# Kernel optimization log

Hardware: AMD Instinct MI355X
Metric: run time of the kernel (lower is better)

Reference implementation:

```python
import jax, jax.numpy as jnp
import numpy as np

EMBED = 1024
HEADS = 16
HEAD_DIM = EMBED // HEADS
BATCH = 2
SEQ = 256

def setup_inputs() -> dict:
    key = jax.random.key(0)
    ks = jax.random.split(key, 6)
    x = jax.random.normal(ks[0], (BATCH, SEQ, EMBED), dtype=jnp.float32)
    s = 1.0 / np.sqrt(HEAD_DIM)
    Wq = jax.random.uniform(ks[1], (HEAD_DIM, HEAD_DIM), jnp.float32, -s, s)
    Wk = jax.random.uniform(ks[2], (HEAD_DIM, HEAD_DIM), jnp.float32, -s, s)
    Wv = jax.random.uniform(ks[3], (HEAD_DIM, HEAD_DIM), jnp.float32, -s, s)
    so = 1.0 / np.sqrt(EMBED)
    Wo = jax.random.uniform(ks[4], (EMBED, EMBED), jnp.float32, -so, so)
    bo = jax.random.uniform(ks[5], (EMBED,), jnp.float32, -so, so)
    return {"x": x, "Wq": Wq, "Wk": Wk, "Wv": Wv, "Wo": Wo, "bo": bo}

def reference(x, Wq, Wk, Wv, Wo, bo):
    n, s, e = x.shape
    xr = x.reshape(n, s, HEADS, HEAD_DIM)          # (n,s,h,d)
    # nn.Linear applies x @ W.T
    q = jnp.einsum('nshd,ed->nshe', xr, Wq)
    k = jnp.einsum('nshd,ed->nshe', xr, Wk)
    v = jnp.einsum('nshd,ed->nshe', xr, Wv)
    # elementwise outer-product score: (n,s,t,h,d), no reduction over d
    energy = q[:, :, None, :, :] * k[:, None, :, :, :]
    # NOTE: original code softmaxes over dim=3 == the HEADS axis
    attn = jax.nn.softmax(energy / jnp.float32(np.sqrt(EMBED)), axis=3)
    out = jnp.einsum('nsthd,nthd->nshd', attn, v)  # reduce over t
    out = out.reshape(n, s, HEADS * HEAD_DIM)
    return out @ Wo.T + bo
```

## Files before the change

kernel.cpp:

```cpp
#include <hip/hip_runtime.h>

#define NB 2
#define SQL 256
#define NH 16
#define HD 64
#define EMB 1024

typedef unsigned short ushortT;
typedef unsigned int uintT;
typedef __attribute__((ext_vector_type(8))) short bf16x8;
typedef __attribute__((ext_vector_type(4))) float f32x4;
typedef __attribute__((ext_vector_type(2))) float f32x2;

__device__ __constant__ float kQSCALE = 1.4426950408889634f / 32.0f;

__device__ __forceinline__ float fexp2(float x) { return __builtin_amdgcn_exp2f(x); }
__device__ __forceinline__ float frcp(float x)  { return __builtin_amdgcn_rcpf(x); }

__device__ __forceinline__ ushortT f2bf(float x) {
    uintT u = __float_as_uint(x);
    u += 0x7fffu + ((u >> 16) & 1u);
    return (ushortT)(u >> 16);
}
__device__ __forceinline__ ushort4 f2bf4(float4 a) {
    return make_ushort4(f2bf(a.x), f2bf(a.y), f2bf(a.z), f2bf(a.w));
}
__device__ __forceinline__ f32x2 unpk2(uintT u) {
    f32x2 r;
    r.x = __uint_as_float(u << 16);
    r.y = __uint_as_float(u & 0xffff0000u);
    return r;
}
__device__ __forceinline__ float pairsum_dpp(float u) {
    const int j = __builtin_amdgcn_mov_dpp(__float_as_int(u), 0xB1, 0xF, 0xF, true);
    return u + __int_as_float(j);
}

__global__ __launch_bounds__(256) void qkv_kernel(
    const float* __restrict__ x,
    const float* __restrict__ Wq,
    const float* __restrict__ Wk,
    const float* __restrict__ Wv,
    const float* __restrict__ Wo,
    ushortT* __restrict__ Q,
    ushortT* __restrict__ K,
    ushortT* __restrict__ V,
    float* __restrict__ AO,
    ushortT* __restrict__ Wob)
{
    __shared__ ushortT wls[3][64 * 72];
    __shared__ ushortT xs[2][16 * 72];

    const int tid = threadIdx.x;
    const int ns0 = blockIdx.x * 2;
    const int g   = blockIdx.x * 256 + tid;

    {
        const float4 z = make_float4(0.f, 0.f, 0.f, 0.f);
        ((float4*)AO)[g] = z;
        ((float4*)AO)[g + 65536] = z;
    }
#pragma unroll
    for (int j = 0; j < 4; ++j) {
        const int f4 = j * 65536 + g;
        ((ushort4*)Wob)[f4] = f2bf4(((const float4*)Wo)[f4]);
    }

#pragma unroll
    for (int m = 0; m < 3; ++m) {
        const float4* src = (m == 0) ? (const float4*)Wq
                          : (m == 1) ? (const float4*)Wk : (const float4*)Wv;
#pragma unroll
        for (int j = 0; j < 4; ++j) {
            const int idx = j * 256 + tid;
            const int e   = idx >> 4;
            const int d4  = idx & 15;
            float4 a = src[idx];
            if (m == 0) { a.x *= kQSCALE; a.y *= kQSCALE; a.z *= kQSCALE; a.w *= kQSCALE; }
            *(ushort4*)&wls[m][e * 72 + d4 * 4] = f2bf4(a);
        }
    }
#pragma unroll
    for (int j = 0; j < 2; ++j) {
        const int idx = j * 256 + tid;
        const int r   = idx >> 8;
        const int h   = (idx >> 4) & 15;
        const int d4  = idx & 15;
        const float4 a = ((const float4*)(x + (size_t)(ns0 + r) * EMB))[idx & 255];
        *(ushort4*)&xs[r][h * 72 + d4 * 4] = f2bf4(a);
    }
    __syncthreads();

    const int w   = tid >> 6;
    const int nsr = w >> 1;
    const int eb0 = (w & 1) * 32;
    const int l   = tid & 63;
    const int lr  = l & 15;
    const int lk  = l >> 4;

    const bf16x8 a0 = *(const bf16x8*)&xs[nsr][lr * 72 + lk * 8];
    const bf16x8 a1 = *(const bf16x8*)&xs[nsr][lr * 72 + 32 + lk * 8];

#pragma unroll
    for (int m = 0; m < 3; ++m) {
        ushortT* outp = (m == 0) ? Q : (m == 1) ? K : V;
#pragma unroll
        for (int ef = 0; ef < 2; ++ef) {
            const int eb = eb0 + ef * 16;
            const bf16x8 b0 = *(const bf16x8*)&wls[m][(eb + lr) * 72 + lk * 8];
            const bf16x8 b1 = *(const bf16x8*)&wls[m][(eb + lr) * 72 + 32 + lk * 8];
            f32x4 c = {0.f, 0.f, 0.f, 0.f};
            c = __builtin_amdgcn_mfma_f32_16x16x32_bf16(a0, b0, c, 0, 0, 0);
            c = __builtin_amdgcn_mfma_f32_16x16x32_bf16(a1, b1, c, 0, 0, 0);
            ushortT* dst = outp + (size_t)(ns0 + nsr) * EMB + (eb + lr) * 16 + lk * 4;
            *(ushort4*)dst = make_ushort4(f2bf(c[0]), f2bf(c[1]), f2bf(c[2]), f2bf(c[3]));
        }
    }
}

#define ATTN_STEP(KU4, VU4)                                                    \
    {                                                                          \
        f32x2 k2[4], v2[4], p0[4], p1[4];                                      \
        k2[0] = unpk2(KU4.x); k2[1] = unpk2(KU4.y);                            \
        k2[2] = unpk2(KU4.z); k2[3] = unpk2(KU4.w);                            \
        _Pragma("unroll")                                                      \
        for (int j = 0; j < 4; ++j) {                                          \
            const f32x2 x0 = q0_2[j] * k2[j];                                  \
            const f32x2 x1 = q1_2[j] * k2[j];                                  \
            p0[j].x = fexp2(x0.x); p0[j].y = fexp2(x0.y);                      \
            p1[j].x = fexp2(x1.x); p1[j].y = fexp2(x1.y);                      \
        }                                                                      \
        const f32x2 s0v = (p0[0] + p0[1]) + (p0[2] + p0[3]);                   \
        const f32x2 s1v = (p1[0] + p1[1]) + (p1[2] + p1[3]);                   \
        const float rs0 = frcp(pairsum_dpp(s0v.x + s0v.y));                    \
        const float rs1 = frcp(pairsum_dpp(s1v.x + s1v.y));                    \
        const f32x2 rb0 = {rs0, rs0};                                          \
        const f32x2 rb1 = {rs1, rs1};                                          \
        v2[0] = unpk2(VU4.x); v2[1] = unpk2(VU4.y);                            \
        v2[2] = unpk2(VU4.z); v2[3] = unpk2(VU4.w);                            \
        _Pragma("unroll")                                                      \
        for (int j = 0; j < 4; ++j) {                                          \
            acc0[j] = __builtin_elementwise_fma(v2[j] * rb0, p0[j], acc0[j]);  \
            acc1[j] = __builtin_elementwise_fma(v2[j] * rb1, p1[j], acc1[j]);  \
        }                                                                      \
    }

__global__ __launch_bounds__(256) void attn_kernel(
    const ushortT* __restrict__ Q,
    const ushortT* __restrict__ K,
    const ushortT* __restrict__ V,
    float* __restrict__ AO)
{
    __shared__ float red[16][256];

    const int b    = blockIdx.x;
    const int tw   = b & 1;
    const int eh   = (b >> 1) & 1;
    const int sg   = (b >> 2) & 127;
    const int n    = b >> 9;
    const int wave = threadIdx.x >> 6;
    const int l    = threadIdx.x & 63;
    const int s0   = sg * 2;
    const int t0   = tw * 128 + wave * 32;

    f32x2 q0_2[4], q1_2[4];
    {
        const uint4* qp = (const uint4*)(Q + (size_t)(n * SQL + s0) * EMB + 512 * eh) + l;
        const uint4 qa = qp[0];
        const uint4 qb = qp[128];
        q0_2[0] = unpk2(qa.x); q0_2[1] = unpk2(qa.y);
        q0_2[2] = unpk2(qa.z); q0_2[3] = unpk2(qa.w);
        q1_2[0] = unpk2(qb.x); q1_2[1] = unpk2(qb.y);
        q1_2[2] = unpk2(qb.z); q1_2[3] = unpk2(qb.w);
    }

    f32x2 acc0[4], acc1[4];
#pragma unroll
    for (int j = 0; j < 4; ++j) {
        acc0[j] = (f32x2){0.f, 0.f};
        acc1[j] = (f32x2){0.f, 0.f};
    }

    const uint4* kp = (const uint4*)(K + (size_t)(n * SQL + t0) * EMB + 512 * eh) + l;
    const uint4* vp = (const uint4*)(V + (size_t)(n * SQL + t0) * EMB + 512 * eh) + l;

    uint4 ka = kp[0];
    uint4 kb = kp[128];
    uint4 va = vp[0];

#pragma unroll
    for (int tt = 0; tt < 30; tt += 2) {
        const uint4 kn2 = kp[256];
        const uint4 vb  = vp[128];
        ATTN_STEP(ka, va);
        const uint4 kn3 = kp[384];
        va = vp[256];
        kp += 256; vp += 256;
        ATTN_STEP(kb, vb);
        ka = kn2; kb = kn3;
    }
    {
        const uint4 vb = vp[128];
        ATTN_STEP(ka, va);
        ATTN_STEP(kb, vb);
    }

#pragma unroll
    for (int j = 0; j < 4; ++j) {
        red[2 * j        ][wave * 64 + l] = acc0[j].x;
        red[2 * j + 1    ][wave * 64 + l] = acc0[j].y;
        red[8 + 2 * j    ][wave * 64 + l] = acc1[j].x;
        red[8 + 2 * j + 1][wave * 64 + l] = acc1[j].y;
    }
    __syncthreads();

    float* aob = AO + (size_t)(n * SQL + s0) * EMB + 512 * (l & 1) + 32 * eh + (l >> 1);
#pragma unroll
    for (int di = 0; di < 4; ++di) {
        const int i = wave * 4 + di;
        const float sum = (red[i][l] + red[i][64 + l]) + (red[i][128 + l] + red[i][192 + l]);
        const int s = i >> 3;
        const int c = i & 7;
        atomicAdd(aob + (size_t)s * EMB + 64 * c, sum);
    }
}

__global__ __launch_bounds__(256) void proj_kernel(
    const float* __restrict__ AO,
    const ushortT* __restrict__ Wob,
    const float* __restrict__ bo,
    float* __restrict__ out)
{
    __shared__ ushortT As[32 * 40];
    __shared__ ushortT Bs[64 * 40];

    const int b  = blockIdx.x;
    const int jt = b & 15;
    const int rt = b >> 4;
    const int tid = threadIdx.x;
    const int r0 = rt * 32, j0 = jt * 64;

    const int w  = tid >> 6;
    const int wr = w >> 1;
    const int wc = w & 1;
    const int l  = tid & 63;
    const int lr = l & 15;
    const int lk = l >> 4;

    const int arow = tid >> 3, akq = tid & 7;
    const int brow = tid >> 2, bko = tid & 3;

    f32x4 c0 = {0.f, 0.f, 0.f, 0.f};
    f32x4 c1 = {0.f, 0.f, 0.f, 0.f};

    float4 aN = *(const float4*)&AO[(size_t)(r0 + arow) * EMB + akq * 4];
    uint4  bN = *(const uint4*)&Wob[(size_t)(j0 + brow) * EMB + bko * 8];

    for (int kt = 0; kt < 32; ++kt) {
        __syncthreads();
        *(ushort4*)&As[arow * 40 + akq * 4] = f2bf4(aN);
        *(uint4*)&Bs[brow * 40 + bko * 8] = bN;
        if (kt < 31) {
            const int kb = (kt + 1) * 32;
            aN = *(const float4*)&AO[(size_t)(r0 + arow) * EMB + kb + akq * 4];
            bN = *(const uint4*)&Wob[(size_t)(j0 + brow) * EMB + kb + bko * 8];
        }
        __syncthreads();

        const bf16x8 a  = *(const bf16x8*)&As[(wr * 16 + lr) * 40 + lk * 8];
        const bf16x8 b0 = *(const bf16x8*)&Bs[(wc * 32 + lr) * 40 + lk * 8];
        const bf16x8 b1 = *(const bf16x8*)&Bs[(wc * 32 + 16 + lr) * 40 + lk * 8];
        c0 = __builtin_amdgcn_mfma_f32_16x16x32_bf16(a, b0, c0, 0, 0, 0);
        c1 = __builtin_amdgcn_mfma_f32_16x16x32_bf16(a, b1, c1, 0, 0, 0);
    }

    const int rbase = r0 + wr * 16 + lk * 4;
    const int jbase = j0 + wc * 32 + lr;
    const float bb0 = bo[jbase];
    const float bb1 = bo[jbase + 16];
#pragma unroll
    for (int e = 0; e < 4; ++e) {
        out[(size_t)(rbase + e) * EMB + jbase]      = c0[e] + bb0;
        out[(size_t)(rbase + e) * EMB + jbase + 16] = c1[e] + bb1;
    }
}

extern "C" void kernel_launch(void* const* d_in, const int* in_sizes, int n_in,
                              void* d_out, int out_size, void* d_ws, size_t ws_size,
                              hipStream_t stream)
{
    const float* x  = (const float*)d_in[0];
    const float* Wq = (const float*)d_in[1];
    const float* Wk = (const float*)d_in[2];
    const float* Wv = (const float*)d_in[3];
    const float* Wo = (const float*)d_in[4];
    const float* bo = (const float*)d_in[5];

    float* ws = (float*)d_ws;
    ushortT* Q   = (ushortT*)ws;
    ushortT* K   = (ushortT*)(ws + 262144);
    ushortT* V   = (ushortT*)(ws + 524288);
    float*   AO  = ws + 786432;
    ushortT* Wob = (ushortT*)(ws + 1310720);

    qkv_kernel<<<256, 256, 0, stream>>>(x, Wq, Wk, Wv, Wo, Q, K, V, AO, Wob);
    attn_kernel<<<1024, 256, 0, stream>>>(Q, K, V, AO);
    proj_kernel<<<256, 256, 0, stream>>>(AO, Wob, bo, (float*)d_out);
}
```

Before: 50.26 us.

## Stage K/V tiles in shared memory shared across waves handling different query rows

Each block now has its four waves handle different query-row pairs over the same 32-key chunk. K/V tiles of 8 rows are staged into double-buffered LDS with register prefetch, so the block reads each K/V row from global memory once instead of once per wave. The per-block LDS reduction is removed: each wave atomically adds its partial sums directly. This raises the global atomic count about fourfold (8 key-chunk blocks instead of 2 per output) and adds LDS traffic plus a barrier per tile, in exchange for less global K/V traffic.

```diff
diff --git a/kernel.cpp b/kernel.cpp
--- a/kernel.cpp
+++ b/kernel.cpp
@@ -151,17 +151,18 @@
     const ushortT* __restrict__ V,
     float* __restrict__ AO)
 {
-    __shared__ float red[16][256];
+    __shared__ ushortT kv[2 * 2 * 8 * 512];
 
     const int b    = blockIdx.x;
-    const int tw   = b & 1;
-    const int eh   = (b >> 1) & 1;
-    const int sg   = (b >> 2) & 127;
+    const int tw   = b & 7;
+    const int eh   = (b >> 3) & 1;
+    const int sg   = (b >> 4) & 31;
     const int n    = b >> 9;
-    const int wave = threadIdx.x >> 6;
-    const int l    = threadIdx.x & 63;
-    const int s0   = sg * 2;
-    const int t0   = tw * 128 + wave * 32;
+    const int tid  = threadIdx.x;
+    const int wave = tid >> 6;
+    const int l    = tid & 63;
+    const int s0   = sg * 8 + wave * 2;
+    const int tB   = tw * 32;
 
     f32x2 q0_2[4], q1_2[4];
     {
@@ -181,47 +182,47 @@
         acc1[j] = (f32x2){0.f, 0.f};
     }
 
-    const uint4* kp = (const uint4*)(K + (size_t)(n * SQL + t0) * EMB + 512 * eh) + l;
-    const uint4* vp = (const uint4*)(V + (size_t)(n * SQL + t0) * EMB + 512 * eh) + l;
-
-    uint4 ka = kp[0];
-    uint4 kb = kp[128];
-    uint4 va = vp[0];
-
-#pragma unroll
-    for (int tt = 0; tt < 30; tt += 2) {
-        const uint4 kn2 = kp[256];
-        const uint4 vb  = vp[128];
-        ATTN_STEP(ka, va);
-        const uint4 kn3 = kp[384];
-        va = vp[256];
-        kp += 256; vp += 256;
-        ATTN_STEP(kb, vb);
-        ka = kn2; kb = kn3;
-    }
-    {
-        const uint4 vb = vp[128];
-        ATTN_STEP(ka, va);
-        ATTN_STEP(kb, vb);
-    }
-
+    const ushortT* Kb = K + (size_t)(n * SQL + tB) * EMB + 512 * eh + l * 8;
+    const ushortT* Vb = V + (size_t)(n * SQL + tB) * EMB + 512 * eh + l * 8;
+    const int rA = wave, rB = 4 + wave;
+
+    uint4 sk0 = *(const uint4*)&Kb[(size_t)rA * EMB];
+    uint4 sk1 = *(const uint4*)&Kb[(size_t)rB * EMB];
+    uint4 sv0 = *(const uint4*)&Vb[(size_t)rA * EMB];
+    uint4 sv1 = *(const uint4*)&Vb[(size_t)rB * EMB];
+
+#pragma unroll
+    for (int tile = 0; tile < 4; ++tile) {
+        const int buf = tile & 1;
+        ushortT* kbuf = &kv[(buf * 2 + 0) * 8 * 512];
+        ushortT* vbuf = &kv[(buf * 2 + 1) * 8 * 512];
+        *(uint4*)&kbuf[rA * 512 + l * 8] = sk0;
+        *(uint4*)&kbuf[rB * 512 + l * 8] = sk1;
+        *(uint4*)&vbuf[rA * 512 + l * 8] = sv0;
+        *(uint4*)&vbuf[rB * 512 + l * 8] = sv1;
+        __syncthreads();
+        if (tile < 3) {
+            const size_t off = (size_t)(tile + 1) * 8 * EMB;
+            sk0 = *(const uint4*)&Kb[off + (size_t)rA * EMB];
+            sk1 = *(const uint4*)&Kb[off + (size_t)rB * EMB];
+            sv0 = *(const uint4*)&Vb[off + (size_t)rA * EMB];
+            sv1 = *(const uint4*)&Vb[off + (size_t)rB * EMB];
+        }
+#pragma unroll
+        for (int t = 0; t < 8; ++t) {
+            const uint4 ku = *(const uint4*)&kbuf[t * 512 + l * 8];
+            const uint4 vu = *(const uint4*)&vbuf[t * 512 + l * 8];
+            ATTN_STEP(ku, vu);
+        }
+    }
+
+    float* aob = AO + (size_t)(n * SQL + s0) * EMB + 512 * (l & 1) + 32 * eh + (l >> 1);
 #pragma unroll
     for (int j = 0; j < 4; ++j) {
-        red[2 * j        ][wave * 64 + l] = acc0[j].x;
-        red[2 * j + 1    ][wave * 64 + l] = acc0[j].y;
-        red[8 + 2 * j    ][wave * 64 + l] = acc1[j].x;
-        red[8 + 2 * j + 1][wave * 64 + l] = acc1[j].y;
-    }
-    __syncthreads();
-
-    float* aob = AO + (size_t)(n * SQL + s0) * EMB + 512 * (l & 1) + 32 * eh + (l >> 1);
-#pragma unroll
-    for (int di = 0; di < 4; ++di) {
-        const int i = wave * 4 + di;
-        const float sum = (red[i][l] + red[i][64 + l]) + (red[i][128 + l] + red[i][192 + l]);
-        const int s = i >> 3;
-        const int c = i & 7;
-        atomicAdd(aob + (size_t)s * EMB + 64 * c, sum);
+        atomicAdd(aob + 64 * (2 * j),           acc0[j].x);
+        atomicAdd(aob + 64 * (2 * j + 1),       acc0[j].y);
+        atomicAdd(aob + EMB + 64 * (2 * j),     acc1[j].x);
+        atomicAdd(aob + EMB + 64 * (2 * j + 1), acc1[j].y);
     }
 }
 
```

Result: slower. 85.78 us (+70.7%).
